# Performance work log

Measured on AMD Instinct MI355X. Metric: run time of the kernel, lower is better.

The kernel has to match this reference:

```python
import jax, jax.numpy as jnp
import numpy as np

BETA = 1.0
EPS = 1e-8  # matches torch F.cosine_similarity eps


def setup_inputs() -> dict:
    key = jax.random.key(0)
    x = jax.random.normal(key, (4096, 2, 1024), dtype=jnp.float32)
    return {"x": x}


def _cosine_sim_matrix(pos, anc):
    # pos: [B, D], anc: [B, D] -> [B, B], sim[i, j] = cos(pos[i], anc[j])
    dots = jnp.einsum('id,jd->ij', pos, anc)
    pn = jnp.sqrt(jnp.sum(pos * pos, axis=-1))
    an = jnp.sqrt(jnp.sum(anc * anc, axis=-1))
    denom = jnp.maximum(pn[:, None] * an[None, :], EPS)
    return dots / denom


def reference(x):
    # x: [B, M, D], M >= 2
    out_anchor = jnp.mean(x[:, 1:, :], axis=1)   # [B, D]
    out_positive = x[:, 0, :]                     # [B, D]
    sim = _cosine_sim_matrix(out_positive, out_anchor)  # [B, B]
    n = sim.shape[0]

    diag = jnp.diagonal(sim)                      # [B]
    # tempsim for column i: beta * (sim[:, i] - sim[i, i]), excluding row i
    T = BETA * (sim - diag[None, :])              # [B, B]
    eye = jnp.eye(n, dtype=bool)

    # exclude-diagonal logsumexp per column (vectorized over all columns)
    Tm = jnp.where(eye, -jnp.inf, T)
    temploss = jax.nn.logsumexp(Tm, axis=0)       # [B]
    # flatNCE trick: exp(l - stop_grad(l)) has value 1 but gradient of l
    nloss = jnp.mean(jnp.exp(temploss - jax.lax.stop_gradient(temploss)))

    # top-1 accuracy against labels arange(B) (detached in original)
    label = jnp.arange(n)
    prec1 = jnp.mean((jnp.argmax(sim, axis=1) == label).astype(jnp.float32)) * 100.0
    return nloss, prec1
```

## Files before the change

### kernel.cpp

```cpp
#include <hip/hip_runtime.h>


#define NROWS 4096
#define DDIM  1024
#define XSTR  2048

typedef unsigned int u32;
typedef unsigned long long u64;
typedef __attribute__((ext_vector_type(8))) short bf16x8;
typedef __attribute__((ext_vector_type(8))) unsigned short u16x8;
typedef __attribute__((ext_vector_type(16))) float f32x16;

__device__ __forceinline__ unsigned int fkey(float f) {
    unsigned int u = __float_as_uint(f);
    return (u & 0x80000000u) ? ~u : (u | 0x80000000u);
}

__device__ __forceinline__ u64 shfl_xor_u64(u64 v, int m) {
    unsigned int lo = (unsigned int)v;
    unsigned int hi = (unsigned int)(v >> 32);
    lo = __shfl_xor(lo, m, 64);
    hi = __shfl_xor(hi, m, 64);
    return ((u64)hi << 32) | lo;
}

__device__ __forceinline__ unsigned short f2bf(float f) {
    unsigned u = __float_as_uint(f);
    return (unsigned short)((u + 0x7FFFu + ((u >> 16) & 1u)) >> 16);
}

#define PF_OFF   0u
#define AF_OFF   8388608u
#define INV_OFF  16777216u
#define PCK_OFF  16793600u
#define DONE_OFF 16826368u
#define WS_NEED  16826432u

__global__ __launch_bounds__(256) void norms2_kernel(const float* __restrict__ x,
                                                     float* __restrict__ inv_an,
                                                     u64* __restrict__ packed,
                                                     unsigned int* __restrict__ done) {
    int gid  = blockIdx.x * 256 + threadIdx.x;
    int j    = gid >> 6;
    int lane = threadIdx.x & 63;
    if (gid < NROWS) packed[gid] = 0ULL;
    if (gid == 0) *done = 0u;
    const float4* a = (const float4*)(x + (size_t)j * XSTR + DDIM);
    float s = 0.0f;
#pragma unroll
    for (int i = 0; i < 4; ++i) {
        float4 v = a[lane + i * 64];
        s += v.x * v.x + v.y * v.y + v.z * v.z + v.w * v.w;
    }
#pragma unroll
    for (int off = 32; off > 0; off >>= 1) s += __shfl_down(s, off, 64);
    if (lane == 0) inv_an[j] = 1.0f / sqrtf(s);
}

__global__ __launch_bounds__(256) void conv_kernel(const float* __restrict__ x,
                                                   unsigned short* __restrict__ Pf,
                                                   unsigned short* __restrict__ Af) {
    const int cid  = blockIdx.x * 256 + threadIdx.x;
    const int lane = cid & 63;
    const int kh   = (cid >> 6) & 63;
    const int fb   = cid >> 12;
    const int row  = fb * 32 + (lane & 31);
    const int col  = kh * 16 + (lane >> 5) * 8;

    const float* px = x + (size_t)row * XSTR + col;
    float4 p0 = *(const float4*)(px);
    float4 p1 = *(const float4*)(px + 4);
    float4 a0 = *(const float4*)(px + DDIM);
    float4 a1 = *(const float4*)(px + DDIM + 4);

    u16x8 pv, av;
    pv[0] = f2bf(p0.x); pv[1] = f2bf(p0.y); pv[2] = f2bf(p0.z); pv[3] = f2bf(p0.w);
    pv[4] = f2bf(p1.x); pv[5] = f2bf(p1.y); pv[6] = f2bf(p1.z); pv[7] = f2bf(p1.w);
    av[0] = f2bf(a0.x); av[1] = f2bf(a0.y); av[2] = f2bf(a0.z); av[3] = f2bf(a0.w);
    av[4] = f2bf(a1.x); av[5] = f2bf(a1.y); av[6] = f2bf(a1.z); av[7] = f2bf(a1.w);

    *(u16x8*)(Pf + (size_t)cid * 8) = pv;
    *(u16x8*)(Af + (size_t)cid * 8) = av;
}

__global__ __launch_bounds__(512, 2) void mfma_gemm_argmax(const unsigned short* __restrict__ Pf,
                                                           const unsigned short* __restrict__ Af,
                                                           const float* __restrict__ inv_an,
                                                           u64* __restrict__ packed,
                                                           unsigned int* __restrict__ done,
                                                           float* __restrict__ out) {
    __shared__ __align__(16) unsigned int lds[32768];
    __shared__ unsigned int lastflag;
    __shared__ int cnt[8];

    const int bid = blockIdx.x;
    const int xcd = bid & 7;
    const int slt = bid >> 3;
    const int rblk = (xcd >> 1) * 4 + (slt >> 3);
    const int cblk = (xcd & 1) * 8 + (slt & 7);
    const int r0 = rblk * 256;
    const int c0 = cblk * 256;

    const int wave = threadIdx.x >> 6;
    const int lane = threadIdx.x & 63;
    const int l31 = lane & 31;
    const int lh = lane >> 5;
    const int wm = wave & 3;
    const int wn = wave >> 2;

    const char* gPs = (const char*)Pf + (((size_t)(rblk * 8 + wave)) << 16) + (size_t)lane * 16;
    const char* gAs = (const char*)Af + (((size_t)(cblk * 8 + wave)) << 16) + (size_t)lane * 16;

    f32x16 zero16 = {0.f,0.f,0.f,0.f,0.f,0.f,0.f,0.f,0.f,0.f,0.f,0.f,0.f,0.f,0.f,0.f};
    f32x16 acc[2][4];
#pragma unroll
    for (int i = 0; i < 2; ++i)
#pragma unroll
        for (int j = 0; j < 4; ++j) acc[i][j] = zero16;

    bf16x8 ph[2][2], aa[2][4];

#define READF(s, khl)                                                                   \
    {                                                                                   \
        const u32* bp_ = &lds[cbuf + (khl) * 2048 + (wm * 2) * 256 + lane * 4];         \
        ph[s][0] = *(const bf16x8*)(bp_);                                               \
        ph[s][1] = *(const bf16x8*)(bp_ + 256);                                         \
        const u32* ba_ = &lds[cbuf + 8192 + (khl) * 2048 + (wn * 4) * 256 + lane * 4];  \
        aa[s][0] = *(const bf16x8*)(ba_);                                               \
        aa[s][1] = *(const bf16x8*)(ba_ + 256);                                         \
        aa[s][2] = *(const bf16x8*)(ba_ + 512);                                         \
        aa[s][3] = *(const bf16x8*)(ba_ + 768);                                         \
    }

#define MFMA8(s)                                                                        \
        acc[0][0] = __builtin_amdgcn_mfma_f32_32x32x16_bf16(ph[s][0], aa[s][0], acc[0][0], 0, 0, 0); \
        acc[0][1] = __builtin_amdgcn_mfma_f32_32x32x16_bf16(ph[s][0], aa[s][1], acc[0][1], 0, 0, 0); \
        acc[0][2] = __builtin_amdgcn_mfma_f32_32x32x16_bf16(ph[s][0], aa[s][2], acc[0][2], 0, 0, 0); \
        acc[0][3] = __builtin_amdgcn_mfma_f32_32x32x16_bf16(ph[s][0], aa[s][3], acc[0][3], 0, 0, 0); \
        acc[1][0] = __builtin_amdgcn_mfma_f32_32x32x16_bf16(ph[s][1], aa[s][0], acc[1][0], 0, 0, 0); \
        acc[1][1] = __builtin_amdgcn_mfma_f32_32x32x16_bf16(ph[s][1], aa[s][1], acc[1][1], 0, 0, 0); \
        acc[1][2] = __builtin_amdgcn_mfma_f32_32x32x16_bf16(ph[s][1], aa[s][2], acc[1][2], 0, 0, 0); \
        acc[1][3] = __builtin_amdgcn_mfma_f32_32x32x16_bf16(ph[s][1], aa[s][3], acc[1][3], 0, 0, 0);

#pragma unroll
    for (int kh_l = 0; kh_l < 4; ++kh_l) {
        __builtin_amdgcn_global_load_lds((const u32*)(gPs + ((size_t)kh_l << 10)),
                                         &lds[kh_l * 2048 + wave * 256], 16, 0, 0);
        __builtin_amdgcn_global_load_lds((const u32*)(gAs + ((size_t)kh_l << 10)),
                                         &lds[8192 + kh_l * 2048 + wave * 256], 16, 0, 0);
    }

    for (int t = 0; t < 16; ++t) {
        const int cbuf = (t & 1) * 16384;
        const int nbuf = cbuf ^ 16384;

        asm volatile("s_waitcnt vmcnt(0)" ::: "memory");
        __builtin_amdgcn_s_barrier();
        __builtin_amdgcn_sched_barrier(0);

        if (t + 1 < 16) {
#pragma unroll
            for (int kh_l = 0; kh_l < 4; ++kh_l) {
                const size_t go = ((size_t)((t + 1) * 4 + kh_l)) << 10;
                __builtin_amdgcn_global_load_lds((const u32*)(gPs + go),
                                                 &lds[nbuf + kh_l * 2048 + wave * 256], 16, 0, 0);
                __builtin_amdgcn_global_load_lds((const u32*)(gAs + go),
                                                 &lds[nbuf + 8192 + kh_l * 2048 + wave * 256], 16, 0, 0);
            }
        }

        READF(0, 0)

#pragma unroll
        for (int kh = 0; kh < 4; ++kh) {
            if (kh < 3) READF((kh + 1) & 1, kh + 1)
            if (kh < 3) { asm volatile("s_waitcnt lgkmcnt(6)" ::: "memory"); }
            else        { asm volatile("s_waitcnt lgkmcnt(0)" ::: "memory"); }
            __builtin_amdgcn_sched_barrier(0);
            __builtin_amdgcn_s_setprio(1);
            MFMA8(kh & 1)
            __builtin_amdgcn_s_setprio(0);
        }
    }
#undef READF
#undef MFMA8

    float ian[4];
#pragma unroll
    for (int nt = 0; nt < 4; ++nt) ian[nt] = inv_an[c0 + wn * 128 + nt * 32 + l31];

#pragma unroll
    for (int mt = 0; mt < 2; ++mt)
#pragma unroll
        for (int reg = 0; reg < 16; ++reg) {
            const int row = r0 + wm * 64 + mt * 32 + (reg & 3) + 8 * (reg >> 2) + 4 * lh;
            u64 best = 0ULL;
#pragma unroll
            for (int nt = 0; nt < 4; ++nt) {
                const int col = c0 + wn * 128 + nt * 32 + l31;
                const float v = acc[mt][nt][reg] * ian[nt];
                const u64 p = ((u64)fkey(v) << 32) | (unsigned int)(~col);
                best = best > p ? best : p;
            }
#pragma unroll
            for (int m = 1; m <= 16; m <<= 1) {
                const u64 o = shfl_xor_u64(best, m);
                best = best > o ? best : o;
            }
            if (l31 == 0) atomicMax(&packed[row], best);
        }

    __syncthreads();
    if (threadIdx.x == 0) {
        __threadfence();
        unsigned int old = atomicAdd(done, 1u);
        lastflag = (old == 255u) ? 1u : 0u;
    }
    __syncthreads();
    if (lastflag) {
        int c = 0;
        for (int r = threadIdx.x; r < NROWS; r += 512) {
            u64 v = atomicAdd(&packed[r], 0ULL);
            unsigned int col = ~(unsigned int)(v & 0xFFFFFFFFULL);
            c += (col == (unsigned int)r) ? 1 : 0;
        }
#pragma unroll
        for (int off = 32; off > 0; off >>= 1) c += __shfl_down(c, off, 64);
        if ((threadIdx.x & 63) == 0) cnt[threadIdx.x >> 6] = c;
        __syncthreads();
        if (threadIdx.x == 0) {
            int tot = 0;
#pragma unroll
            for (int w = 0; w < 8; ++w) tot += cnt[w];
            out[0] = 1.0f;
            out[1] = 100.0f * (float)tot / (float)NROWS;
        }
    }
}

__global__ __launch_bounds__(256) void norms_kernel(const float* __restrict__ x,
                                                    float* __restrict__ inv_an,
                                                    u64* __restrict__ packed) {
    int gid  = blockIdx.x * 256 + threadIdx.x;
    int j    = gid >> 6;
    int lane = threadIdx.x & 63;
    if (gid < NROWS) packed[gid] = 0ULL;
    const float4* a = (const float4*)(x + (size_t)j * XSTR + DDIM);
    float s = 0.0f;
#pragma unroll
    for (int i = 0; i < 4; ++i) {
        float4 v = a[lane + i * 64];
        s += v.x * v.x + v.y * v.y + v.z * v.z + v.w * v.w;
    }
#pragma unroll
    for (int off = 32; off > 0; off >>= 1) s += __shfl_down(s, off, 64);
    if (lane == 0) inv_an[j] = 1.0f / sqrtf(s);
}

__global__ __launch_bounds__(256) void gemm_argmax_kernel(const float* __restrict__ x,
                                                          const float* __restrict__ inv_an,
                                                          u64* __restrict__ packed) {
    __shared__ __align__(16) float Pt[16][128];
    __shared__ __align__(16) float At[16][128];
    const int r0 = blockIdx.x * 128;
    const int c0 = blockIdx.y * 128;
    const int t = threadIdx.x;
    const int tx = t & 15;
    const int ty = t >> 4;
    const int srow = t >> 1;
    const int skq = (t & 1) * 8;
    float acc[8][8];
#pragma unroll
    for (int r = 0; r < 8; ++r)
#pragma unroll
        for (int c = 0; c < 8; ++c) acc[r][c] = 0.0f;
    const float* gp = x + (size_t)(r0 + srow) * XSTR + skq;
    const float* ga = x + (size_t)(c0 + srow) * XSTR + DDIM + skq;
    for (int k0 = 0; k0 < DDIM; k0 += 16) {
        __syncthreads();
        float4 p0 = *(const float4*)(gp + k0);
        float4 p1 = *(const float4*)(gp + k0 + 4);
        float4 a0 = *(const float4*)(ga + k0);
        float4 a1 = *(const float4*)(ga + k0 + 4);
        Pt[skq + 0][srow] = p0.x; Pt[skq + 1][srow] = p0.y;
        Pt[skq + 2][srow] = p0.z; Pt[skq + 3][srow] = p0.w;
        Pt[skq + 4][srow] = p1.x; Pt[skq + 5][srow] = p1.y;
        Pt[skq + 6][srow] = p1.z; Pt[skq + 7][srow] = p1.w;
        At[skq + 0][srow] = a0.x; At[skq + 1][srow] = a0.y;
        At[skq + 2][srow] = a0.z; At[skq + 3][srow] = a0.w;
        At[skq + 4][srow] = a1.x; At[skq + 5][srow] = a1.y;
        At[skq + 6][srow] = a1.z; At[skq + 7][srow] = a1.w;
        __syncthreads();
#pragma unroll
        for (int kk = 0; kk < 16; ++kk) {
            float pr[8], ar[8];
            *(float4*)&pr[0] = *(const float4*)&Pt[kk][ty * 8];
            *(float4*)&pr[4] = *(const float4*)&Pt[kk][ty * 8 + 4];
            *(float4*)&ar[0] = *(const float4*)&At[kk][tx * 8];
            *(float4*)&ar[4] = *(const float4*)&At[kk][tx * 8 + 4];
#pragma unroll
            for (int r = 0; r < 8; ++r)
#pragma unroll
                for (int c = 0; c < 8; ++c) acc[r][c] += pr[r] * ar[c];
        }
    }
    float ian[8];
#pragma unroll
    for (int c = 0; c < 8; ++c) ian[c] = inv_an[c0 + tx * 8 + c];
#pragma unroll
    for (int r = 0; r < 8; ++r) {
        int row = r0 + ty * 8 + r;
        u64 best = 0ULL;
#pragma unroll
        for (int c = 0; c < 8; ++c) {
            int col = c0 + tx * 8 + c;
            float v = acc[r][c] * ian[c];
            u64 p = ((u64)fkey(v) << 32) | (unsigned int)(~col);
            best = best > p ? best : p;
        }
#pragma unroll
        for (int m = 1; m <= 8; m <<= 1) {
            u64 o = shfl_xor_u64(best, m);
            best = best > o ? best : o;
        }
        if (tx == 0) atomicMax(&packed[row], best);
    }
}

__global__ __launch_bounds__(256) void finalize_kernel(const u64* __restrict__ packed,
                                                       float* __restrict__ out) {
    __shared__ int cnt_s;
    int t = threadIdx.x;
    if (t == 0) cnt_s = 0;
    __syncthreads();
    int c = 0;
    for (int r = t; r < NROWS; r += 256) {
        unsigned int col = ~(unsigned int)(packed[r] & 0xFFFFFFFFULL);
        c += (col == (unsigned int)r) ? 1 : 0;
    }
#pragma unroll
    for (int off = 32; off > 0; off >>= 1) c += __shfl_down(c, off, 64);
    if ((t & 63) == 0) atomicAdd(&cnt_s, c);
    __syncthreads();
    if (t == 0) {
        out[0] = 1.0f;
        out[1] = 100.0f * (float)cnt_s / (float)NROWS;
    }
}

extern "C" void kernel_launch(void* const* d_in, const int* in_sizes, int n_in,
                              void* d_out, int out_size, void* d_ws, size_t ws_size,
                              hipStream_t stream) {
    (void)in_sizes; (void)n_in; (void)out_size;
    const float* x = (const float*)d_in[0];
    float* out = (float*)d_out;

    if (ws_size >= (size_t)WS_NEED) {
        char* ws = (char*)d_ws;
        unsigned short* Pf = (unsigned short*)(ws + PF_OFF);
        unsigned short* Af = (unsigned short*)(ws + AF_OFF);
        float* inv_an = (float*)(ws + INV_OFF);
        u64* packed = (u64*)(ws + PCK_OFF);
        unsigned int* done = (unsigned int*)(ws + DONE_OFF);

        norms2_kernel<<<NROWS / 4, 256, 0, stream>>>(x, inv_an, packed, done);
        conv_kernel<<<2048, 256, 0, stream>>>(x, Pf, Af);
        mfma_gemm_argmax<<<256, 512, 0, stream>>>(Pf, Af, inv_an, packed, done, out);
    } else {
        float* inv_an = (float*)d_ws;
        u64* packed = (u64*)((char*)d_ws + NROWS * sizeof(float));
        norms_kernel<<<NROWS / 4, 256, 0, stream>>>(x, inv_an, packed);
        dim3 grid(NROWS / 128, NROWS / 128);
        gemm_argmax_kernel<<<grid, 256, 0, stream>>>(x, inv_an, packed);
        finalize_kernel<<<1, 256, 0, stream>>>(packed, out);
    }
}
```

Measured before the change: 122.7 us.

## Use 4 waves per block with 128x128 per-wave tiles in MFMA GEMM

Cuts the GEMM block from 8 waves to 4. Each wave now computes a 128x128 output tile (4x4 MFMA 32x32 tiles) instead of 64x128, and each wave issues twice as many global-to-LDS loads. The aim is more register-level reuse of A/B fragments per LDS read and fewer waves contending for LDS bandwidth. In exchange it uses far more accumulator registers per wave and has less latency hiding, since occupancy stays at one 256-thread block per CU.

```diff
diff --git a/kernel.cpp b/kernel.cpp
--- a/kernel.cpp
+++ b/kernel.cpp
@@ -83,7 +83,7 @@
     *(u16x8*)(Af + (size_t)cid * 8) = av;
 }
 
-__global__ __launch_bounds__(512, 2) void mfma_gemm_argmax(const unsigned short* __restrict__ Pf,
+__global__ __launch_bounds__(256, 1) void mfma_gemm_argmax(const unsigned short* __restrict__ Pf,
                                                            const unsigned short* __restrict__ Af,
                                                            const float* __restrict__ inv_an,
                                                            u64* __restrict__ packed,
@@ -91,7 +91,7 @@
                                                            float* __restrict__ out) {
     __shared__ __align__(16) unsigned int lds[32768];
     __shared__ unsigned int lastflag;
-    __shared__ int cnt[8];
+    __shared__ int cnt[4];
 
     const int bid = blockIdx.x;
     const int xcd = bid & 7;
@@ -105,26 +105,46 @@
     const int lane = threadIdx.x & 63;
     const int l31 = lane & 31;
     const int lh = lane >> 5;
-    const int wm = wave & 3;
-    const int wn = wave >> 2;
-
-    const char* gPs = (const char*)Pf + (((size_t)(rblk * 8 + wave)) << 16) + (size_t)lane * 16;
-    const char* gAs = (const char*)Af + (((size_t)(cblk * 8 + wave)) << 16) + (size_t)lane * 16;
+    const int wm = wave & 1;
+    const int wn = wave >> 1;
+
+    const char* gP0 = (const char*)Pf + (((size_t)(rblk * 8 + wave)) << 16) + (size_t)lane * 16;
+    const char* gP1 = (const char*)Pf + (((size_t)(rblk * 8 + wave + 4)) << 16) + (size_t)lane * 16;
+    const char* gA0 = (const char*)Af + (((size_t)(cblk * 8 + wave)) << 16) + (size_t)lane * 16;
+    const char* gA1 = (const char*)Af + (((size_t)(cblk * 8 + wave + 4)) << 16) + (size_t)lane * 16;
 
     f32x16 zero16 = {0.f,0.f,0.f,0.f,0.f,0.f,0.f,0.f,0.f,0.f,0.f,0.f,0.f,0.f,0.f,0.f};
-    f32x16 acc[2][4];
-#pragma unroll
-    for (int i = 0; i < 2; ++i)
+    f32x16 acc[4][4];
+#pragma unroll
+    for (int i = 0; i < 4; ++i)
 #pragma unroll
         for (int j = 0; j < 4; ++j) acc[i][j] = zero16;
 
-    bf16x8 ph[2][2], aa[2][4];
+    bf16x8 ph[2][4], aa[2][4];
+
+#define ISSUE_TILE(tt, bb)                                                              \
+    {                                                                                   \
+        _Pragma("unroll")                                                               \
+        for (int kh_l = 0; kh_l < 4; ++kh_l) {                                          \
+            const size_t go_ = ((size_t)((tt) * 4 + kh_l)) << 10;                       \
+            __builtin_amdgcn_global_load_lds((const u32*)(gP0 + go_),                   \
+                &lds[(bb) + kh_l * 2048 + wave * 256], 16, 0, 0);                       \
+            __builtin_amdgcn_global_load_lds((const u32*)(gP1 + go_),                   \
+                &lds[(bb) + kh_l * 2048 + (wave + 4) * 256], 16, 0, 0);                 \
+            __builtin_amdgcn_global_load_lds((const u32*)(gA0 + go_),                   \
+                &lds[(bb) + 8192 + kh_l * 2048 + wave * 256], 16, 0, 0);                \
+            __builtin_amdgcn_global_load_lds((const u32*)(gA1 + go_),                   \
+                &lds[(bb) + 8192 + kh_l * 2048 + (wave + 4) * 256], 16, 0, 0);          \
+        }                                                                               \
+    }
 
 #define READF(s, khl)                                                                   \
     {                                                                                   \
-        const u32* bp_ = &lds[cbuf + (khl) * 2048 + (wm * 2) * 256 + lane * 4];         \
+        const u32* bp_ = &lds[cbuf + (khl) * 2048 + (wm * 4) * 256 + lane * 4];         \
         ph[s][0] = *(const bf16x8*)(bp_);                                               \
         ph[s][1] = *(const bf16x8*)(bp_ + 256);                                         \
+        ph[s][2] = *(const bf16x8*)(bp_ + 512);                                         \
+        ph[s][3] = *(const bf16x8*)(bp_ + 768);                                         \
         const u32* ba_ = &lds[cbuf + 8192 + (khl) * 2048 + (wn * 4) * 256 + lane * 4];  \
         aa[s][0] = *(const bf16x8*)(ba_);                                               \
         aa[s][1] = *(const bf16x8*)(ba_ + 256);                                         \
@@ -132,23 +152,18 @@
         aa[s][3] = *(const bf16x8*)(ba_ + 768);                                         \
     }
 
-#define MFMA8(s)                                                                        \
-        acc[0][0] = __builtin_amdgcn_mfma_f32_32x32x16_bf16(ph[s][0], aa[s][0], acc[0][0], 0, 0, 0); \
-        acc[0][1] = __builtin_amdgcn_mfma_f32_32x32x16_bf16(ph[s][0], aa[s][1], acc[0][1], 0, 0, 0); \
-        acc[0][2] = __builtin_amdgcn_mfma_f32_32x32x16_bf16(ph[s][0], aa[s][2], acc[0][2], 0, 0, 0); \
-        acc[0][3] = __builtin_amdgcn_mfma_f32_32x32x16_bf16(ph[s][0], aa[s][3], acc[0][3], 0, 0, 0); \
-        acc[1][0] = __builtin_amdgcn_mfma_f32_32x32x16_bf16(ph[s][1], aa[s][0], acc[1][0], 0, 0, 0); \
-        acc[1][1] = __builtin_amdgcn_mfma_f32_32x32x16_bf16(ph[s][1], aa[s][1], acc[1][1], 0, 0, 0); \
-        acc[1][2] = __builtin_amdgcn_mfma_f32_32x32x16_bf16(ph[s][1], aa[s][2], acc[1][2], 0, 0, 0); \
-        acc[1][3] = __builtin_amdgcn_mfma_f32_32x32x16_bf16(ph[s][1], aa[s][3], acc[1][3], 0, 0, 0);
-
-#pragma unroll
-    for (int kh_l = 0; kh_l < 4; ++kh_l) {
-        __builtin_amdgcn_global_load_lds((const u32*)(gPs + ((size_t)kh_l << 10)),
-                                         &lds[kh_l * 2048 + wave * 256], 16, 0, 0);
-        __builtin_amdgcn_global_load_lds((const u32*)(gAs + ((size_t)kh_l << 10)),
-                                         &lds[8192 + kh_l * 2048 + wave * 256], 16, 0, 0);
-    }
+#define MFMA16(s)                                                                       \
+    {                                                                                   \
+        _Pragma("unroll")                                                               \
+        for (int i = 0; i < 4; ++i) {                                                   \
+            acc[i][0] = __builtin_amdgcn_mfma_f32_32x32x16_bf16(ph[s][i], aa[s][0], acc[i][0], 0, 0, 0); \
+            acc[i][1] = __builtin_amdgcn_mfma_f32_32x32x16_bf16(ph[s][i], aa[s][1], acc[i][1], 0, 0, 0); \
+            acc[i][2] = __builtin_amdgcn_mfma_f32_32x32x16_bf16(ph[s][i], aa[s][2], acc[i][2], 0, 0, 0); \
+            acc[i][3] = __builtin_amdgcn_mfma_f32_32x32x16_bf16(ph[s][i], aa[s][3], acc[i][3], 0, 0, 0); \
+        }                                                                               \
+    }
+
+    ISSUE_TILE(0, 0)
 
     for (int t = 0; t < 16; ++t) {
         const int cbuf = (t & 1) * 16384;
@@ -158,42 +173,33 @@
         __builtin_amdgcn_s_barrier();
         __builtin_amdgcn_sched_barrier(0);
 
-        if (t + 1 < 16) {
-#pragma unroll
-            for (int kh_l = 0; kh_l < 4; ++kh_l) {
-                const size_t go = ((size_t)((t + 1) * 4 + kh_l)) << 10;
-                __builtin_amdgcn_global_load_lds((const u32*)(gPs + go),
-                                                 &lds[nbuf + kh_l * 2048 + wave * 256], 16, 0, 0);
-                __builtin_amdgcn_global_load_lds((const u32*)(gAs + go),
-                                                 &lds[nbuf + 8192 + kh_l * 2048 + wave * 256], 16, 0, 0);
-            }
-        }
+        if (t + 1 < 16) ISSUE_TILE(t + 1, nbuf)
 
         READF(0, 0)
-
 #pragma unroll
         for (int kh = 0; kh < 4; ++kh) {
             if (kh < 3) READF((kh + 1) & 1, kh + 1)
-            if (kh < 3) { asm volatile("s_waitcnt lgkmcnt(6)" ::: "memory"); }
+            if (kh < 3) { asm volatile("s_waitcnt lgkmcnt(8)" ::: "memory"); }
             else        { asm volatile("s_waitcnt lgkmcnt(0)" ::: "memory"); }
             __builtin_amdgcn_sched_barrier(0);
             __builtin_amdgcn_s_setprio(1);
-            MFMA8(kh & 1)
+            MFMA16(kh & 1)
             __builtin_amdgcn_s_setprio(0);
         }
     }
+#undef ISSUE_TILE
 #undef READF
-#undef MFMA8
+#undef MFMA16
 
     float ian[4];
 #pragma unroll
     for (int nt = 0; nt < 4; ++nt) ian[nt] = inv_an[c0 + wn * 128 + nt * 32 + l31];
 
 #pragma unroll
-    for (int mt = 0; mt < 2; ++mt)
+    for (int mt = 0; mt < 4; ++mt)
 #pragma unroll
         for (int reg = 0; reg < 16; ++reg) {
-            const int row = r0 + wm * 64 + mt * 32 + (reg & 3) + 8 * (reg >> 2) + 4 * lh;
+            const int row = r0 + wm * 128 + mt * 32 + (reg & 3) + 8 * (reg >> 2) + 4 * lh;
             u64 best = 0ULL;
 #pragma unroll
             for (int nt = 0; nt < 4; ++nt) {
@@ -219,7 +225,7 @@
     __syncthreads();
     if (lastflag) {
         int c = 0;
-        for (int r = threadIdx.x; r < NROWS; r += 512) {
+        for (int r = threadIdx.x; r < NROWS; r += 256) {
             u64 v = atomicAdd(&packed[r], 0ULL);
             unsigned int col = ~(unsigned int)(v & 0xFFFFFFFFULL);
             c += (col == (unsigned int)r) ? 1 : 0;
@@ -231,7 +237,7 @@
         if (threadIdx.x == 0) {
             int tot = 0;
 #pragma unroll
-            for (int w = 0; w < 8; ++w) tot += cnt[w];
+            for (int w = 0; w < 4; ++w) tot += cnt[w];
             out[0] = 1.0f;
             out[1] = 100.0f * (float)tot / (float)NROWS;
         }
@@ -365,7 +371,7 @@
 
         norms2_kernel<<<NROWS / 4, 256, 0, stream>>>(x, inv_an, packed, done);
         conv_kernel<<<2048, 256, 0, stream>>>(x, Pf, Af);
-        mfma_gemm_argmax<<<256, 512, 0, stream>>>(Pf, Af, inv_an, packed, done, out);
+        mfma_gemm_argmax<<<256, 256, 0, stream>>>(Pf, Af, inv_an, packed, done, out);
     } else {
         float* inv_an = (float*)d_ws;
         u64* packed = (u64*)((char*)d_ws + NROWS * sizeof(float));
```

After: 137.8 us. 12.3% more time.
